# Kernel tuning notes

Measured on AMD Instinct MI355X. Metric: run time of the kernel, lower is better.

Reference implementation:

```python
import jax, jax.numpy as jnp
import numpy as np

B, T, D = 2, 1024, 128
NEG_INF = -1e9


def setup_inputs() -> dict:
    key = jax.random.key(0)
    k_h, k_m, k_w = jax.random.split(key, 3)
    h = jax.random.normal(k_h, (B, T, D), dtype=jnp.float32)
    mask = jax.random.uniform(k_m, (B, T)) < 0.9  # bool [B, T]
    w = jax.random.normal(k_w, (D,), dtype=jnp.float32) * (1.0 / np.sqrt(D))  # Linear(dim,1,bias=False)
    return {"h": h, "mask": mask, "w": w}


def reference(h, mask, w):
    # wj[b, j] = W(h[b, j]) : score column scale, independent of i
    wj = jnp.einsum("btd,d->bt", h, w)  # [B, T]
    # pairwise L1 distance: dist[b, i, j] = sum_d |h[b,i,d] - h[b,j,d]|
    dist = jnp.abs(h[:, :, None, :] - h[:, None, :, :]).sum(-1)  # [B, T, T]
    score = -wj[:, None, :] * dist  # [B, T, T]
    score = jnp.where(mask[:, None, :], score, NEG_INF)
    alpha = jax.nn.softmax(score, axis=-1)  # [B, T, T]
    ctx = jnp.einsum("bij,bjd->bid", alpha, h)  # [B, T, D]
    return jnp.concatenate([h, ctx], axis=-1)  # [B, T, 2D]
```

## Files before the change

kernel.cpp:

```cpp
#include <hip/hip_runtime.h>
#include <math.h>

#define TT 1024
#define DD 128

static constexpr float kNegInf = -1e9f;

typedef __fp16 h2 __attribute__((ext_vector_type(2)));

__device__ __forceinline__ unsigned int pk16(float a, float b) {
  h2 v = __builtin_amdgcn_cvt_pkrtz(a, b);
  return __builtin_bit_cast(unsigned int, v);
}
__device__ __forceinline__ float dot2f(unsigned int a, unsigned int b, float c) {
#if __has_builtin(__builtin_amdgcn_fdot2)
  return __builtin_amdgcn_fdot2(__builtin_bit_cast(h2, a),
                                __builtin_bit_cast(h2, b), c, false);
#else
  h2 av = __builtin_bit_cast(h2, a), bv = __builtin_bit_cast(h2, b);
  return c + (float)av.x * (float)bv.x + (float)av.y * (float)bv.y;
#endif
}

__global__ __launch_bounds__(256) void k_prep(const float* __restrict__ h,
                                              const float* __restrict__ w,
                                              const int* __restrict__ mk,
                                              float* __restrict__ hTf,
                                              unsigned int* __restrict__ hT16,
                                              float* __restrict__ swj,
                                              float* __restrict__ bias) {
  __shared__ __align__(16) float tile[32][132];
  __shared__ float wred[32][8];
  const int b  = blockIdx.x >> 5;
  const int jt = blockIdx.x & 31;
  const int tid = threadIdx.x;
  const float4* src = (const float4*)h + (size_t)(b * TT + jt * 32) * 32;
#pragma unroll
  for (int k = 0; k < 4; ++k) {
    int idx = k * 256 + tid;
    float4 v = src[idx];
    int j = idx >> 5, c = idx & 31;
    *((float4*)&tile[j][c * 4]) = v;
  }
  __syncthreads();
#pragma unroll
  for (int k = 0; k < 4; ++k) {
    int idx = k * 256 + tid;
    int d = idx >> 3, jq = idx & 7;
    float4 v = {tile[jq * 4 + 0][d], tile[jq * 4 + 1][d],
                tile[jq * 4 + 2][d], tile[jq * 4 + 3][d]};
    *(float4*)&hTf[(size_t)(b * DD + d) * TT + jt * 32 + jq * 4] = v;
  }
#pragma unroll
  for (int k = 0; k < 2; ++k) {
    int idx = k * 256 + tid;
    int jp = idx >> 5, dq = idx & 31;
    uint4 wv;
    wv.x = pk16(tile[jp * 2][dq * 4 + 0], tile[jp * 2 + 1][dq * 4 + 0]);
    wv.y = pk16(tile[jp * 2][dq * 4 + 1], tile[jp * 2 + 1][dq * 4 + 1]);
    wv.z = pk16(tile[jp * 2][dq * 4 + 2], tile[jp * 2 + 1][dq * 4 + 2]);
    wv.w = pk16(tile[jp * 2][dq * 4 + 3], tile[jp * 2 + 1][dq * 4 + 3]);
    *(uint4*)&hT16[((size_t)(b * 512 + jt * 16 + jp)) * DD + dq * 4] = wv;
  }
  {
    const int j = tid & 31, dg = tid >> 5;
    float p = 0.f;
#pragma unroll
    for (int e = 0; e < 16; e += 4) {
      float4 hv = *(const float4*)&tile[j][dg * 16 + e];
      float4 wv = *(const float4*)&w[dg * 16 + e];
      p += hv.x * wv.x + hv.y * wv.y + hv.z * wv.z + hv.w * wv.w;
    }
    wred[j][dg] = p;
  }
  __syncthreads();
  if (tid < 32) {
    const int row = b * TT + jt * 32 + tid;
    float a = 0.f;
#pragma unroll
    for (int e = 0; e < 8; ++e) a += wred[tid][e];
    const bool ok = (mk[row] != 0);
    swj[row]  = ok ? -a : 0.f;
    bias[row] = ok ? 0.f : kNegInf;
  }
}

__global__ __launch_bounds__(512, 2) void k_fused(
    const float* __restrict__ h, const float* __restrict__ hTf,
    const unsigned int* __restrict__ hT16,
    const float* __restrict__ swj, const float* __restrict__ bias,
    float* __restrict__ out) {
  __shared__ __align__(16) float A_lds[8][DD];
  __shared__ __align__(16) unsigned int Pt[512][8];
  __shared__ __align__(16) float ctxp[4][8][DD];
  __shared__ float redm[8][4];
  __shared__ float redl[8][4];

  const int tid  = threadIdx.x;
  const int lane = tid & 63;
  const int wv   = tid >> 6;
  const int rh   = tid >> 8;
  const int b    = blockIdx.x >> 7;
  const int row0 = (blockIdx.x & 127) * 8;
  const int rot  = blockIdx.x & 31;

  {
    const float2 v = *(const float2*)(h + ((size_t)b * TT + row0) * DD + tid * 2);
    *(float2*)&A_lds[0][tid * 2] = v;
  }
  __syncthreads();

  const int q = tid & 255;
  const int j = q * 4;
  const float* Bb = hTf + (size_t)b * DD * TT + j;
  const int ar = rh * 4;
  float acc[4][4];
#pragma unroll
  for (int u = 0; u < 4; ++u)
#pragma unroll
    for (int r = 0; r < 4; ++r) acc[u][r] = 0.f;

#define PS(s) (((s) + rot) & 31)

#define LOADB4(B, s) {                                        \
    B[0] = *(const float4*)(Bb + (size_t)((s) * 4 + 0) * TT); \
    B[1] = *(const float4*)(Bb + (size_t)((s) * 4 + 1) * TT); \
    B[2] = *(const float4*)(Bb + (size_t)((s) * 4 + 2) * TT); \
    B[3] = *(const float4*)(Bb + (size_t)((s) * 4 + 3) * TT); }

#define COMP4(B, s) {                                                  \
    _Pragma("unroll") for (int r = 0; r < 4; ++r) {                    \
      const float4 Ar = *(const float4*)&A_lds[ar + r][(s) * 4];       \
      _Pragma("unroll") for (int e = 0; e < 4; ++e) {                  \
        const float a = (e == 0) ? Ar.x : (e == 1) ? Ar.y              \
                        : (e == 2) ? Ar.z : Ar.w;                      \
        acc[0][r] += fabsf(a - B[e].x);                                \
        acc[1][r] += fabsf(a - B[e].y);                                \
        acc[2][r] += fabsf(a - B[e].z);                                \
        acc[3][r] += fabsf(a - B[e].w);                                \
      } } }

  {
    float4 B0[4], B1[4];
    LOADB4(B0, PS(0));
#pragma unroll 1
    for (int s = 0; s < 16; ++s) {
      const int p1 = PS(2 * s + 1);
      const int p0 = PS(2 * s);
      LOADB4(B1, p1);
      COMP4(B0, p0);
      if (s < 15) LOADB4(B0, PS(2 * s + 2));
      COMP4(B1, p1);
    }
  }

  const float4 swv = *(const float4*)(swj + (size_t)b * TT + j);
  const float4 bvv = *(const float4*)(bias + (size_t)b * TT + j);
  float sc[4][4];
#pragma unroll
  for (int r = 0; r < 4; ++r) {
    sc[0][r] = fmaf(swv.x, acc[0][r], bvv.x);
    sc[1][r] = fmaf(swv.y, acc[1][r], bvv.y);
    sc[2][r] = fmaf(swv.z, acc[2][r], bvv.z);
    sc[3][r] = fmaf(swv.w, acc[3][r], bvv.w);
  }

  {
    float mr[4];
#pragma unroll
    for (int r = 0; r < 4; ++r) {
      float m0 = fmaxf(fmaxf(sc[0][r], sc[1][r]), fmaxf(sc[2][r], sc[3][r]));
#pragma unroll
      for (int off = 32; off; off >>= 1) m0 = fmaxf(m0, __shfl_xor(m0, off));
      mr[r] = m0;
    }
    if (lane == 0) {
#pragma unroll
      for (int r = 0; r < 4; ++r) redm[wv][r] = mr[r];
    }
  }
  __syncthreads();
  float M[4];
#pragma unroll
  for (int r = 0; r < 4; ++r)
    M[r] = fmaxf(fmaxf(redm[rh * 4 + 0][r], redm[rh * 4 + 1][r]),
                 fmaxf(redm[rh * 4 + 2][r], redm[rh * 4 + 3][r]));

  {
    float p[4][4];
    float ls[4] = {0.f, 0.f, 0.f, 0.f};
#pragma unroll
    for (int u = 0; u < 4; ++u)
#pragma unroll
      for (int r = 0; r < 4; ++r) {
        p[u][r] = __expf(sc[u][r] - M[r]);
        ls[r] += p[u][r];
      }
    uint4 w0 = {pk16(p[0][0], p[1][0]), pk16(p[0][1], p[1][1]),
                pk16(p[0][2], p[1][2]), pk16(p[0][3], p[1][3])};
    uint4 w1 = {pk16(p[2][0], p[3][0]), pk16(p[2][1], p[3][1]),
                pk16(p[2][2], p[3][2]), pk16(p[2][3], p[3][3])};
    *(uint4*)&Pt[2 * q + 0][rh * 4] = w0;
    *(uint4*)&Pt[2 * q + 1][rh * 4] = w1;
#pragma unroll
    for (int r = 0; r < 4; ++r) {
#pragma unroll
      for (int off = 32; off; off >>= 1) ls[r] += __shfl_xor(ls[r], off);
    }
    if (lane == 0) {
#pragma unroll
      for (int r = 0; r < 4; ++r) redl[wv][r] = ls[r];
    }
  }
  __syncthreads();

  const int dp  = tid & 63;
  const int rh2 = (tid >> 6) & 1;
  const int s   = tid >> 7;
  const unsigned int* Vp =
      hT16 + ((size_t)(b * 512 + s * 128)) * DD + dp * 2;
  float cx[4][2];
#pragma unroll
  for (int r = 0; r < 4; ++r) { cx[r][0] = 0.f; cx[r][1] = 0.f; }
  const int qrot = rot * 4;
#pragma unroll 4
  for (int qq = 0; qq < 128; ++qq) {
    const int qi = (qq + qrot) & 127;
    const uint4 P = *(const uint4*)&Pt[s * 128 + qi][rh2 * 4];
    const uint2 V = *(const uint2*)(Vp + (size_t)qi * DD);
    cx[0][0] = dot2f(P.x, V.x, cx[0][0]); cx[0][1] = dot2f(P.x, V.y, cx[0][1]);
    cx[1][0] = dot2f(P.y, V.x, cx[1][0]); cx[1][1] = dot2f(P.y, V.y, cx[1][1]);
    cx[2][0] = dot2f(P.z, V.x, cx[2][0]); cx[2][1] = dot2f(P.z, V.y, cx[2][1]);
    cx[3][0] = dot2f(P.w, V.x, cx[3][0]); cx[3][1] = dot2f(P.w, V.y, cx[3][1]);
  }
#pragma unroll
  for (int r = 0; r < 4; ++r)
    *(float2*)&ctxp[s][rh2 * 4 + r][dp * 2] = make_float2(cx[r][0], cx[r][1]);
  __syncthreads();

#pragma unroll
  for (int k = 0; k < 2; ++k) {
    const int idx = tid + k * 512;
    const int r = idx >> 7, d = idx & 127;
    const int hb = (r >> 2) * 4, rr = r & 3;
    const float L = redl[hb + 0][rr] + redl[hb + 1][rr] +
                    redl[hb + 2][rr] + redl[hb + 3][rr];
    const float c = (ctxp[0][r][d] + ctxp[1][r][d]) +
                    (ctxp[2][r][d] + ctxp[3][r][d]);
    const size_t row = (size_t)blockIdx.x * 8 + r;
    out[row * 256 + d]       = A_lds[r][d];
    out[row * 256 + 128 + d] = c / L;
  }
}

extern "C" void kernel_launch(void* const* d_in, const int* in_sizes, int n_in,
                              void* d_out, int out_size, void* d_ws, size_t ws_size,
                              hipStream_t stream) {
  const float* h  = (const float*)d_in[0];
  const int*   mk = (const int*)d_in[1];
  const float* w  = (const float*)d_in[2];
  float* out = (float*)d_out;

  char* ws = (char*)d_ws;
  float*        swj  = (float*)ws;
  float*        bias = (float*)(ws + 8192);
  float*        hTf  = (float*)(ws + 16384);
  unsigned int* hT16 = (unsigned int*)(ws + 16384 + 1048576);

  hipLaunchKernelGGL(k_prep,  dim3(64),  dim3(256), 0, stream,
                     h, w, mk, hTf, hT16, swj, bias);
  hipLaunchKernelGGL(k_fused, dim3(256), dim3(512), 0, stream,
                     h, hTf, hT16, swj, bias, out);
}
```

Baseline: 40.31 us.

## Compute pairwise L1 distances in packed fp16 with abs-mask and dot2 reduction

Stores the transposed copy of h as packed fp16 pairs along D and converts the query rows to fp16. The distance loop uses packed half subtraction, a sign-bit mask and fdot2 against ones to accumulate |a-b| in fp32. This halves the memory traffic for B and cuts the ALU instruction count per element pair. The identity half of the output is now read from global h instead of LDS. Distances lose precision to fp16 rounding, and since softmax scores are scaled by wj this could change results noticeably.

```diff
diff --git a/kernel.cpp b/kernel.cpp
--- a/kernel.cpp
+++ b/kernel.cpp
@@ -10,6 +10,10 @@
 
 __device__ __forceinline__ unsigned int pk16(float a, float b) {
   h2 v = __builtin_amdgcn_cvt_pkrtz(a, b);
+  return __builtin_bit_cast(unsigned int, v);
+}
+__device__ __forceinline__ unsigned int pkrne(float a, float b) {
+  h2 v; v.x = (__fp16)a; v.y = (__fp16)b;
   return __builtin_bit_cast(unsigned int, v);
 }
 __device__ __forceinline__ float dot2f(unsigned int a, unsigned int b, float c) {
@@ -21,11 +25,16 @@
   return c + (float)av.x * (float)bv.x + (float)av.y * (float)bv.y;
 #endif
 }
+__device__ __forceinline__ float absdot(unsigned int a, unsigned int b, float c) {
+  h2 d = __builtin_bit_cast(h2, a) - __builtin_bit_cast(h2, b);
+  unsigned int ad = __builtin_bit_cast(unsigned int, d) & 0x7FFF7FFFu;
+  return dot2f(ad, 0x3C003C00u, c);
+}
 
 __global__ __launch_bounds__(256) void k_prep(const float* __restrict__ h,
                                               const float* __restrict__ w,
                                               const int* __restrict__ mk,
-                                              float* __restrict__ hTf,
+                                              unsigned int* __restrict__ hTd16,
                                               unsigned int* __restrict__ hT16,
                                               float* __restrict__ swj,
                                               float* __restrict__ bias) {
@@ -44,12 +53,11 @@
   }
   __syncthreads();
 #pragma unroll
-  for (int k = 0; k < 4; ++k) {
+  for (int k = 0; k < 8; ++k) {
     int idx = k * 256 + tid;
-    int d = idx >> 3, jq = idx & 7;
-    float4 v = {tile[jq * 4 + 0][d], tile[jq * 4 + 1][d],
-                tile[jq * 4 + 2][d], tile[jq * 4 + 3][d]};
-    *(float4*)&hTf[(size_t)(b * DD + d) * TT + jt * 32 + jq * 4] = v;
+    int d2 = idx >> 5, jl = idx & 31;
+    hTd16[((size_t)(b * 64 + d2)) * TT + jt * 32 + jl] =
+        pkrne(tile[jl][2 * d2], tile[jl][2 * d2 + 1]);
   }
 #pragma unroll
   for (int k = 0; k < 2; ++k) {
@@ -86,11 +94,11 @@
 }
 
 __global__ __launch_bounds__(512, 2) void k_fused(
-    const float* __restrict__ h, const float* __restrict__ hTf,
+    const float* __restrict__ h, const unsigned int* __restrict__ hTd16,
     const unsigned int* __restrict__ hT16,
     const float* __restrict__ swj, const float* __restrict__ bias,
     float* __restrict__ out) {
-  __shared__ __align__(16) float A_lds[8][DD];
+  __shared__ __align__(16) unsigned int A16[8][64];
   __shared__ __align__(16) unsigned int Pt[512][8];
   __shared__ __align__(16) float ctxp[4][8][DD];
   __shared__ float redm[8][4];
@@ -102,17 +110,19 @@
   const int rh   = tid >> 8;
   const int b    = blockIdx.x >> 7;
   const int row0 = (blockIdx.x & 127) * 8;
-  const int rot  = blockIdx.x & 31;
-
-  {
-    const float2 v = *(const float2*)(h + ((size_t)b * TT + row0) * DD + tid * 2);
-    *(float2*)&A_lds[0][tid * 2] = v;
+  const int rot  = blockIdx.x & 15;
+
+  {
+    const int r = tid >> 6, d2 = tid & 63;
+    const float2 av =
+        *(const float2*)(h + ((size_t)b * TT + row0 + r) * DD + 2 * d2);
+    A16[r][d2] = pkrne(av.x, av.y);
   }
   __syncthreads();
 
   const int q = tid & 255;
   const int j = q * 4;
-  const float* Bb = hTf + (size_t)b * DD * TT + j;
+  const unsigned int* Bb = hTd16 + (size_t)b * 64 * TT + j;
   const int ar = rh * 4;
   float acc[4][4];
 #pragma unroll
@@ -120,37 +130,37 @@
 #pragma unroll
     for (int r = 0; r < 4; ++r) acc[u][r] = 0.f;
 
-#define PS(s) (((s) + rot) & 31)
-
-#define LOADB4(B, s) {                                        \
-    B[0] = *(const float4*)(Bb + (size_t)((s) * 4 + 0) * TT); \
-    B[1] = *(const float4*)(Bb + (size_t)((s) * 4 + 1) * TT); \
-    B[2] = *(const float4*)(Bb + (size_t)((s) * 4 + 2) * TT); \
-    B[3] = *(const float4*)(Bb + (size_t)((s) * 4 + 3) * TT); }
-
-#define COMP4(B, s) {                                                  \
+#define PS(s) (((s) + rot) & 15)
+
+#define LOADB16(B, s) {                                       \
+    B[0] = *(const uint4*)(Bb + (size_t)((s) * 4 + 0) * TT);  \
+    B[1] = *(const uint4*)(Bb + (size_t)((s) * 4 + 1) * TT);  \
+    B[2] = *(const uint4*)(Bb + (size_t)((s) * 4 + 2) * TT);  \
+    B[3] = *(const uint4*)(Bb + (size_t)((s) * 4 + 3) * TT); }
+
+#define COMP16(B, s) {                                                 \
     _Pragma("unroll") for (int r = 0; r < 4; ++r) {                    \
-      const float4 Ar = *(const float4*)&A_lds[ar + r][(s) * 4];       \
-      _Pragma("unroll") for (int e = 0; e < 4; ++e) {                  \
-        const float a = (e == 0) ? Ar.x : (e == 1) ? Ar.y              \
-                        : (e == 2) ? Ar.z : Ar.w;                      \
-        acc[0][r] += fabsf(a - B[e].x);                                \
-        acc[1][r] += fabsf(a - B[e].y);                                \
-        acc[2][r] += fabsf(a - B[e].z);                                \
-        acc[3][r] += fabsf(a - B[e].w);                                \
+      const uint4 aw = *(const uint4*)&A16[ar + r][(s) * 4];           \
+      _Pragma("unroll") for (int dl = 0; dl < 4; ++dl) {               \
+        const unsigned int a = (dl == 0) ? aw.x : (dl == 1) ? aw.y     \
+                               : (dl == 2) ? aw.z : aw.w;              \
+        acc[0][r] = absdot(a, B[dl].x, acc[0][r]);                     \
+        acc[1][r] = absdot(a, B[dl].y, acc[1][r]);                     \
+        acc[2][r] = absdot(a, B[dl].z, acc[2][r]);                     \
+        acc[3][r] = absdot(a, B[dl].w, acc[3][r]);                     \
       } } }
 
   {
-    float4 B0[4], B1[4];
-    LOADB4(B0, PS(0));
+    uint4 B0[4], B1[4];
+    LOADB16(B0, PS(0));
 #pragma unroll 1
-    for (int s = 0; s < 16; ++s) {
+    for (int s = 0; s < 8; ++s) {
       const int p1 = PS(2 * s + 1);
       const int p0 = PS(2 * s);
-      LOADB4(B1, p1);
-      COMP4(B0, p0);
-      if (s < 15) LOADB4(B0, PS(2 * s + 2));
-      COMP4(B1, p1);
+      LOADB16(B1, p1);
+      COMP16(B0, p0);
+      if (s < 7) LOADB16(B0, PS(2 * s + 2));
+      COMP16(B1, p1);
     }
   }
 
@@ -222,7 +232,7 @@
   float cx[4][2];
 #pragma unroll
   for (int r = 0; r < 4; ++r) { cx[r][0] = 0.f; cx[r][1] = 0.f; }
-  const int qrot = rot * 4;
+  const int qrot = rot * 8;
 #pragma unroll 4
   for (int qq = 0; qq < 128; ++qq) {
     const int qi = (qq + qrot) & 127;
@@ -248,7 +258,7 @@
     const float c = (ctxp[0][r][d] + ctxp[1][r][d]) +
                     (ctxp[2][r][d] + ctxp[3][r][d]);
     const size_t row = (size_t)blockIdx.x * 8 + r;
-    out[row * 256 + d]       = A_lds[r][d];
+    out[row * 256 + d]       = h[row * DD + d];
     out[row * 256 + 128 + d] = c / L;
   }
 }
@@ -262,13 +272,13 @@
   float* out = (float*)d_out;
 
   char* ws = (char*)d_ws;
-  float*        swj  = (float*)ws;
-  float*        bias = (float*)(ws + 8192);
-  float*        hTf  = (float*)(ws + 16384);
-  unsigned int* hT16 = (unsigned int*)(ws + 16384 + 1048576);
+  float*        swj   = (float*)ws;
+  float*        bias  = (float*)(ws + 8192);
+  unsigned int* hTd16 = (unsigned int*)(ws + 16384);
+  unsigned int* hT16  = (unsigned int*)(ws + 16384 + 524288);
 
   hipLaunchKernelGGL(k_prep,  dim3(64),  dim3(256), 0, stream,
-                     h, w, mk, hTf, hT16, swj, bias);
+                     h, w, mk, hTd16, hT16, swj, bias);
   hipLaunchKernelGGL(k_fused, dim3(256), dim3(512), 0, stream,
-                     h, hTf, hT16, swj, bias, out);
-}
+                     h, hTd16, hT16, swj, bias, out);
+}
```

New measurement: 35.40 us. -12.2%, faster.
